# Optimization experiments

Hardware: AMD Instinct MI355X
Metric: run time of the kernel (lower is better)

The kernel has to match this reference:

```python
import jax, jax.numpy as jnp
import numpy as np

B, N, K, D, H = 8, 128, 64, 256, 8  # batch, groups, keys-per-query, k_dim (=h_size), n_head


def setup_inputs() -> dict:
    key = jax.random.key(0)
    kq, kk, kv, kw, kb = jax.random.split(key, 5)
    bound = 1.0 / np.sqrt(D)  # torch nn.Bilinear default init bound
    return {
        "q": jax.random.normal(kq, (B, N, 1, D), jnp.float32),
        "k": jax.random.normal(kk, (B, N, K, D), jnp.float32),
        "v": jax.random.normal(kv, (B, N, K, D), jnp.float32),
        "W": jax.random.uniform(kw, (H, D, D), jnp.float32, -bound, bound),
        "b": jax.random.uniform(kb, (H,), jnp.float32, -bound, bound),
    }


def reference(q, k, v, W, b):
    Bs, Ns, Ks, Ds = k.shape
    Hh = W.shape[0]
    qe = q[:, :, 0, :]  # (B,N,D); torch expands q over K, einsum broadcasts instead
    # nn.Bilinear: scores[b,n,k,h] = q[b,n,:] @ W[h] @ k[b,n,k,:] + b[h]
    scores = jnp.einsum('bnd,hde,bnke->bnkh', qe, W, k) + b  # (B,N,K,H)
    # Faithful to torch's .view(B, N, -1, K): row-major reinterpretation of the
    # trailing (K, H) pair as (H, K) — a dim-mixing reshape, not a transpose.
    attn = scores.reshape(Bs, Ns, Hh, Ks)
    attn = jax.nn.softmax(attn, axis=-1)  # softmax over last dim (dropout p=0)
    # matmul(attn, v) -> (B,N,H,Dv); then sum over the head axis
    output = jnp.einsum('bnhk,bnkd->bnd', attn, v)
    return output, attn
```

## Files before the change

### kernel.cpp

```cpp
#include <hip/hip_runtime.h>
#include <math.h>

namespace {

constexpr int D = 256;
constexpr int H = 8;

typedef __attribute__((ext_vector_type(8))) short bf16x8;
typedef __attribute__((ext_vector_type(4))) float f32x4;

__device__ inline unsigned short bf16rn(float x) {
  unsigned u = __builtin_bit_cast(unsigned, x);
  u += 0x7fffu + ((u >> 16) & 1u);
  return (unsigned short)(u >> 16);
}
__device__ inline float bf16tof(unsigned short b) {
  return __builtin_bit_cast(float, (unsigned)b << 16);
}

constexpr size_t OFF_QWB = 0;
constexpr size_t OFF_WFH = (size_t)8 << 20;
constexpr size_t OFF_WFL = (size_t)9 << 20;
constexpr size_t OFF_QFH = (size_t)10 << 20;
constexpr size_t OFF_QFL = ((size_t)10 << 20) + ((size_t)512 << 10);

__global__ __launch_bounds__(256) void prep_kernel(
    const float* __restrict__ q, const float* __restrict__ W,
    char* __restrict__ ws) {
  const int gid = blockIdx.x * 256 + threadIdx.x;
  float e[8];
  char *hi_base, *lo_base;
  size_t outoff;
  if (gid < 65536) {
    const int l = gid & 63, ks = (gid >> 6) & 7, he = gid >> 9;
    const int h = he >> 4, et = he & 15;
    const int d0 = ks * 32 + ((l >> 4) << 3);
    const int ecol = et * 16 + (l & 15);
    const float* src = W + (size_t)h * 65536 + (size_t)d0 * 256 + ecol;
    #pragma unroll
    for (int j = 0; j < 8; ++j) e[j] = src[j * 256];
    hi_base = ws + OFF_WFH; lo_base = ws + OFF_WFL;
    outoff = (size_t)gid * 16;
  } else {
    const int t = gid - 65536;
    const int l = t & 63, ks = (t >> 6) & 7, bt = t >> 9;
    const int row = bt * 16 + (l & 15);
    const int d0 = ks * 32 + ((l >> 4) << 3);
    const float4* src = reinterpret_cast<const float4*>(q + (size_t)row * 256 + d0);
    float4 a = src[0], b = src[1];
    e[0] = a.x; e[1] = a.y; e[2] = a.z; e[3] = a.w;
    e[4] = b.x; e[5] = b.y; e[6] = b.z; e[7] = b.w;
    hi_base = ws + OFF_QFH; lo_base = ws + OFF_QFL;
    outoff = (size_t)t * 16;
  }
  unsigned hw[4], lw[4];
  #pragma unroll
  for (int p = 0; p < 4; ++p) {
    unsigned short h0 = bf16rn(e[2 * p]), h1 = bf16rn(e[2 * p + 1]);
    unsigned short l0 = bf16rn(e[2 * p] - bf16tof(h0));
    unsigned short l1 = bf16rn(e[2 * p + 1] - bf16tof(h1));
    hw[p] = (unsigned)h0 | ((unsigned)h1 << 16);
    lw[p] = (unsigned)l0 | ((unsigned)l1 << 16);
  }
  *reinterpret_cast<uint4*>(hi_base + outoff) = make_uint4(hw[0], hw[1], hw[2], hw[3]);
  *reinterpret_cast<uint4*>(lo_base + outoff) = make_uint4(lw[0], lw[1], lw[2], lw[3]);
}

__global__ __launch_bounds__(256) void qw_mfma_kernel(
    const char* __restrict__ ws_in, unsigned short* __restrict__ qWb) {
  const int tid = threadIdx.x;
  const int w   = blockIdx.x * 4 + (tid >> 6);
  const int l   = tid & 63;
  const int bng = w >> 5;
  const int heg = w & 31;
  const char* qfh = ws_in + OFF_QFH;
  const char* qfl = ws_in + OFF_QFL;
  const char* wfh = ws_in + OFF_WFH;
  const char* wfl = ws_in + OFF_WFL;

  f32x4 acc[2][4];
  #pragma unroll
  for (int i = 0; i < 2; ++i)
    #pragma unroll
    for (int j = 0; j < 4; ++j) acc[i][j] = {0.f, 0.f, 0.f, 0.f};

  #pragma unroll 2
  for (int ks = 0; ks < 8; ++ks) {
    bf16x8 aH[2], aL[2], bH[4], bL[4];
    #pragma unroll
    for (int i = 0; i < 2; ++i) {
      const size_t off = ((size_t)((bng * 2 + i) * 8 + ks) * 64 + l) * 16;
      aH[i] = *reinterpret_cast<const bf16x8*>(qfh + off);
      aL[i] = *reinterpret_cast<const bf16x8*>(qfl + off);
    }
    #pragma unroll
    for (int j = 0; j < 4; ++j) {
      const size_t off = ((size_t)((heg * 4 + j) * 8 + ks) * 64 + l) * 16;
      bH[j] = *reinterpret_cast<const bf16x8*>(wfh + off);
      bL[j] = *reinterpret_cast<const bf16x8*>(wfl + off);
    }
    #pragma unroll
    for (int i = 0; i < 2; ++i)
      #pragma unroll
      for (int j = 0; j < 4; ++j) {
        acc[i][j] = __builtin_amdgcn_mfma_f32_16x16x32_bf16(aH[i], bH[j], acc[i][j], 0, 0, 0);
        acc[i][j] = __builtin_amdgcn_mfma_f32_16x16x32_bf16(aH[i], bL[j], acc[i][j], 0, 0, 0);
        acc[i][j] = __builtin_amdgcn_mfma_f32_16x16x32_bf16(aL[i], bH[j], acc[i][j], 0, 0, 0);
      }
  }

  const int rbase = (l >> 4) * 4;
  const int col   = l & 15;
  #pragma unroll
  for (int i = 0; i < 2; ++i)
    #pragma unroll
    for (int j = 0; j < 4; ++j) {
      const size_t cidx = (size_t)(heg * 4 + j) * 16 + col;
      #pragma unroll
      for (int r = 0; r < 4; ++r) {
        const int bn = (bng * 2 + i) * 16 + rbase + r;
        qWb[(size_t)bn * 2048 + cidx] = bf16rn(acc[i][j][r]);
      }
    }
}

constexpr int FB2   = 0;
constexpr int WSP2  = 8320;
constexpr int SMEM3 = 9344;

__global__ __launch_bounds__(256, 4) void attn_fused_kernel(
    const unsigned short* __restrict__ qWb, const float* __restrict__ kin,
    const float* __restrict__ vin, const float* __restrict__ bin,
    float* __restrict__ out, float* __restrict__ attn_out) {
  __shared__ alignas(16) long long smem_ll[SMEM3 / 8];
  char* sm = reinterpret_cast<char*>(smem_ll);
  float* wsp = reinterpret_cast<float*>(sm + WSP2);
  const int tid = threadIdx.x;
  const int bn  = blockIdx.x;
  const int wid = tid >> 6;
  const int ln  = tid & 63;

  const float* arow = kin + (size_t)bn * 16384 +
                      (size_t)(wid * 16 + (ln & 15)) * 256 + ((ln >> 4) << 3);
  float4 ka[16];
  #pragma unroll
  for (int ks = 0; ks < 8; ++ks) {
    ka[2 * ks]     = *reinterpret_cast<const float4*>(arow + ks * 32);
    ka[2 * ks + 1] = *reinterpret_cast<const float4*>(arow + ks * 32 + 4);
  }
  uint4 qh = *reinterpret_cast<const uint4*>(qWb + (size_t)bn * 2048 + tid * 8);

  {
    const int ks = tid >> 5, slot = 32 + (tid & 31);
    *reinterpret_cast<uint4*>(sm + FB2 + ks * 1040 + slot * 16) =
        make_uint4(0u, 0u, 0u, 0u);
  }
  #pragma unroll
  for (int i = 0; i < 2; ++i) {
    const int p = 2 * tid + i;
    const int hh = p >> 6, equad = p & 63;
    const int ks = equad >> 3, g = (equad >> 1) & 3, j0 = (equad & 1) * 4;
    const int base = FB2 + ks * 1040 + (hh * 4 + g) * 16 + j0 * 2;
    *reinterpret_cast<uint2*>(sm + base) =
        i == 0 ? make_uint2(qh.x, qh.y) : make_uint2(qh.z, qh.w);
  }
  __syncthreads();

  const int slot_r = (ln & 15) * 4 + (ln >> 4);
  const char* pbH = sm + FB2 + slot_r * 16;
  f32x4 acc = {0.f, 0.f, 0.f, 0.f};
  #pragma unroll
  for (int ks = 0; ks < 8; ++ks) {
    const float4 a0 = ka[2 * ks], a1 = ka[2 * ks + 1];
    bf16x8 aH;
    aH[0] = (short)bf16rn(a0.x); aH[1] = (short)bf16rn(a0.y);
    aH[2] = (short)bf16rn(a0.z); aH[3] = (short)bf16rn(a0.w);
    aH[4] = (short)bf16rn(a1.x); aH[5] = (short)bf16rn(a1.y);
    aH[6] = (short)bf16rn(a1.z); aH[7] = (short)bf16rn(a1.w);
    bf16x8 bH = *reinterpret_cast<const bf16x8*>(pbH + ks * 1040);
    acc = __builtin_amdgcn_mfma_f32_16x16x32_bf16(aH, bH, acc, 0, 0, 0);
  }

  const float bias = bin[ln & 7];
  const int col = ln & 15;
  const bool valid = col < 8;
  float x0 = acc[0] + bias, x1 = acc[1] + bias, x2 = acc[2] + bias, x3 = acc[3] + bias;
  float m = valid ? fmaxf(fmaxf(x0, x1), fmaxf(x2, x3)) : -1e30f;
  m = fmaxf(m, __shfl_xor(m, 1, 64));
  m = fmaxf(m, __shfl_xor(m, 2, 64));
  m = fmaxf(m, __shfl_xor(m, 4, 64));
  m = fmaxf(m, __shfl_xor(m, 16, 64));
  float e0 = valid ? expf(x0 - m) : 0.f;
  float e1 = valid ? expf(x1 - m) : 0.f;
  float e2 = valid ? expf(x2 - m) : 0.f;
  float e3 = valid ? expf(x3 - m) : 0.f;
  float s = e0 + e1 + e2 + e3;
  s += __shfl_xor(s, 1, 64);
  s += __shfl_xor(s, 2, 64);
  s += __shfl_xor(s, 4, 64);
  s += __shfl_xor(s, 16, 64);
  float inv = 1.f / s;
  float p0 = e0 * inv, p1 = e1 * inv, p2 = e2 * inv, p3 = e3 * inv;
  if (valid) {
    size_t base = (size_t)bn * 512 + (size_t)(wid * 16 + (ln >> 4) * 4) * 8 + col;
    attn_out[base]      = p0;
    attn_out[base + 8]  = p1;
    attn_out[base + 16] = p2;
    attn_out[base + 24] = p3;
  }
  p0 += __shfl_xor(p0, 32, 64);
  p1 += __shfl_xor(p1, 32, 64);
  p2 += __shfl_xor(p2, 32, 64);
  p3 += __shfl_xor(p3, 32, 64);
  if (ln < 32 && (ln & 15) < 8) {
    const int rb = (ln >> 4) * 4;
    const int c8 = ln & 7;
    float* w = wsp + wid * 64;
    w[(rb + 0) * 8 + c8] = p0;
    w[(rb + 1) * 8 + c8] = p1;
    w[(rb + 2) * 8 + c8] = p2;
    w[(rb + 3) * 8 + c8] = p3;
  }
  __syncthreads();

  const float4* v4 = reinterpret_cast<const float4*>(vin) + (size_t)bn * 4096;
  float4 av = make_float4(0.f, 0.f, 0.f, 0.f);
  #pragma unroll
  for (int i = 0; i < 16; ++i) {
    const int r = wid + 4 * i;
    float w = wsp[r] + wsp[64 + r] + wsp[128 + r] + wsp[192 + r];
    float4 vv = v4[r * 64 + ln];
    av.x += w * vv.x; av.y += w * vv.y; av.z += w * vv.z; av.w += w * vv.w;
  }
  float* s_red = reinterpret_cast<float*>(sm);
  *reinterpret_cast<float4*>(&s_red[wid * 260 + (ln << 2)]) = av;
  __syncthreads();

  out[(size_t)bn * D + tid] =
      s_red[tid] + s_red[260 + tid] + s_red[520 + tid] + s_red[780 + tid];
}

}

extern "C" void kernel_launch(void* const* d_in, const int* in_sizes, int n_in,
                              void* d_out, int out_size, void* d_ws, size_t ws_size,
                              hipStream_t stream) {
  const float* q = (const float*)d_in[0];
  const float* k = (const float*)d_in[1];
  const float* v = (const float*)d_in[2];
  const float* W = (const float*)d_in[3];
  const float* b = (const float*)d_in[4];

  float* out  = (float*)d_out;
  float* attn = out + 262144;
  char*  ws   = (char*)d_ws;
  unsigned short* qWb = (unsigned short*)(ws + OFF_QWB);

  hipLaunchKernelGGL(prep_kernel,       dim3(384),  dim3(256), 0, stream, q, W, ws);
  hipLaunchKernelGGL(qw_mfma_kernel,    dim3(256),  dim3(256), 0, stream, ws, qWb);
  hipLaunchKernelGGL(attn_fused_kernel, dim3(1024), dim3(256), 0, stream,
                     qWb, k, v, b, out, attn);
}
```

Baseline: 41.43 us.

## Fuse bf16 hi/lo split of q and W into the qW MFMA kernel

Removes the separate prep kernel that wrote bf16 hi/lo fragment layouts of q and W to the workspace. The MFMA kernel now loads fp32 q and W directly and splits them into hi/lo in registers, with a smaller per-wave tile (1x2 instead of 2x4) over a four-times larger grid. This saves one launch and a workspace round trip. In exchange, W is re-read and re-converted by many more waves, using strided scalar fp32 loads.

```diff
diff --git a/kernel.cpp b/kernel.cpp
--- a/kernel.cpp
+++ b/kernel.cpp
@@ -17,111 +17,72 @@
 __device__ inline float bf16tof(unsigned short b) {
   return __builtin_bit_cast(float, (unsigned)b << 16);
 }
-
-constexpr size_t OFF_QWB = 0;
-constexpr size_t OFF_WFH = (size_t)8 << 20;
-constexpr size_t OFF_WFL = (size_t)9 << 20;
-constexpr size_t OFF_QFH = (size_t)10 << 20;
-constexpr size_t OFF_QFL = ((size_t)10 << 20) + ((size_t)512 << 10);
-
-__global__ __launch_bounds__(256) void prep_kernel(
+__device__ inline void hilo8(const float* e, bf16x8& hv, bf16x8& lv) {
+  #pragma unroll
+  for (int p = 0; p < 8; ++p) {
+    unsigned short h = bf16rn(e[p]);
+    hv[p] = (short)h;
+    lv[p] = (short)bf16rn(e[p] - bf16tof(h));
+  }
+}
+
+__global__ __launch_bounds__(256) void qw_direct_kernel(
     const float* __restrict__ q, const float* __restrict__ W,
-    char* __restrict__ ws) {
-  const int gid = blockIdx.x * 256 + threadIdx.x;
-  float e[8];
-  char *hi_base, *lo_base;
-  size_t outoff;
-  if (gid < 65536) {
-    const int l = gid & 63, ks = (gid >> 6) & 7, he = gid >> 9;
-    const int h = he >> 4, et = he & 15;
-    const int d0 = ks * 32 + ((l >> 4) << 3);
-    const int ecol = et * 16 + (l & 15);
-    const float* src = W + (size_t)h * 65536 + (size_t)d0 * 256 + ecol;
-    #pragma unroll
-    for (int j = 0; j < 8; ++j) e[j] = src[j * 256];
-    hi_base = ws + OFF_WFH; lo_base = ws + OFF_WFL;
-    outoff = (size_t)gid * 16;
-  } else {
-    const int t = gid - 65536;
-    const int l = t & 63, ks = (t >> 6) & 7, bt = t >> 9;
-    const int row = bt * 16 + (l & 15);
-    const int d0 = ks * 32 + ((l >> 4) << 3);
-    const float4* src = reinterpret_cast<const float4*>(q + (size_t)row * 256 + d0);
-    float4 a = src[0], b = src[1];
-    e[0] = a.x; e[1] = a.y; e[2] = a.z; e[3] = a.w;
-    e[4] = b.x; e[5] = b.y; e[6] = b.z; e[7] = b.w;
-    hi_base = ws + OFF_QFH; lo_base = ws + OFF_QFL;
-    outoff = (size_t)t * 16;
-  }
-  unsigned hw[4], lw[4];
-  #pragma unroll
-  for (int p = 0; p < 4; ++p) {
-    unsigned short h0 = bf16rn(e[2 * p]), h1 = bf16rn(e[2 * p + 1]);
-    unsigned short l0 = bf16rn(e[2 * p] - bf16tof(h0));
-    unsigned short l1 = bf16rn(e[2 * p + 1] - bf16tof(h1));
-    hw[p] = (unsigned)h0 | ((unsigned)h1 << 16);
-    lw[p] = (unsigned)l0 | ((unsigned)l1 << 16);
-  }
-  *reinterpret_cast<uint4*>(hi_base + outoff) = make_uint4(hw[0], hw[1], hw[2], hw[3]);
-  *reinterpret_cast<uint4*>(lo_base + outoff) = make_uint4(lw[0], lw[1], lw[2], lw[3]);
-}
-
-__global__ __launch_bounds__(256) void qw_mfma_kernel(
-    const char* __restrict__ ws_in, unsigned short* __restrict__ qWb) {
+    unsigned short* __restrict__ qWb) {
   const int tid = threadIdx.x;
   const int w   = blockIdx.x * 4 + (tid >> 6);
   const int l   = tid & 63;
-  const int bng = w >> 5;
-  const int heg = w & 31;
-  const char* qfh = ws_in + OFF_QFH;
-  const char* qfl = ws_in + OFF_QFL;
-  const char* wfh = ws_in + OFF_WFH;
-  const char* wfl = ws_in + OFF_WFL;
-
-  f32x4 acc[2][4];
-  #pragma unroll
-  for (int i = 0; i < 2; ++i)
-    #pragma unroll
-    for (int j = 0; j < 4; ++j) acc[i][j] = {0.f, 0.f, 0.f, 0.f};
+  const int bt  = w >> 6;
+  const int hp  = w & 63;
+  const int lrow  = l & 15;
+  const int lcol8 = (l >> 4) << 3;
+
+  f32x4 acc[2];
+  acc[0] = f32x4{0.f, 0.f, 0.f, 0.f};
+  acc[1] = f32x4{0.f, 0.f, 0.f, 0.f};
+
+  const float* qbase = q + (size_t)(bt * 16 + lrow) * 256 + lcol8;
 
   #pragma unroll 2
   for (int ks = 0; ks < 8; ++ks) {
-    bf16x8 aH[2], aL[2], bH[4], bL[4];
+    float ea[8];
+    {
+      const float4 a0 = *reinterpret_cast<const float4*>(qbase + ks * 32);
+      const float4 a1 = *reinterpret_cast<const float4*>(qbase + ks * 32 + 4);
+      ea[0] = a0.x; ea[1] = a0.y; ea[2] = a0.z; ea[3] = a0.w;
+      ea[4] = a1.x; ea[5] = a1.y; ea[6] = a1.z; ea[7] = a1.w;
+    }
+    bf16x8 aH, aL;
+    hilo8(ea, aH, aL);
+
     #pragma unroll
-    for (int i = 0; i < 2; ++i) {
-      const size_t off = ((size_t)((bng * 2 + i) * 8 + ks) * 64 + l) * 16;
-      aH[i] = *reinterpret_cast<const bf16x8*>(qfh + off);
-      aL[i] = *reinterpret_cast<const bf16x8*>(qfl + off);
+    for (int j = 0; j < 2; ++j) {
+      const int he = hp * 2 + j;
+      const int h  = he >> 4, et = he & 15;
+      const float* wp = W + (size_t)h * 65536 +
+                        (size_t)(ks * 32 + lcol8) * 256 + et * 16 + lrow;
+      float eb[8];
+      #pragma unroll
+      for (int jj = 0; jj < 8; ++jj) eb[jj] = wp[(size_t)jj * 256];
+      bf16x8 bH, bL;
+      hilo8(eb, bH, bL);
+      acc[j] = __builtin_amdgcn_mfma_f32_16x16x32_bf16(aH, bH, acc[j], 0, 0, 0);
+      acc[j] = __builtin_amdgcn_mfma_f32_16x16x32_bf16(aH, bL, acc[j], 0, 0, 0);
+      acc[j] = __builtin_amdgcn_mfma_f32_16x16x32_bf16(aL, bH, acc[j], 0, 0, 0);
     }
-    #pragma unroll
-    for (int j = 0; j < 4; ++j) {
-      const size_t off = ((size_t)((heg * 4 + j) * 8 + ks) * 64 + l) * 16;
-      bH[j] = *reinterpret_cast<const bf16x8*>(wfh + off);
-      bL[j] = *reinterpret_cast<const bf16x8*>(wfl + off);
-    }
-    #pragma unroll
-    for (int i = 0; i < 2; ++i)
-      #pragma unroll
-      for (int j = 0; j < 4; ++j) {
-        acc[i][j] = __builtin_amdgcn_mfma_f32_16x16x32_bf16(aH[i], bH[j], acc[i][j], 0, 0, 0);
-        acc[i][j] = __builtin_amdgcn_mfma_f32_16x16x32_bf16(aH[i], bL[j], acc[i][j], 0, 0, 0);
-        acc[i][j] = __builtin_amdgcn_mfma_f32_16x16x32_bf16(aL[i], bH[j], acc[i][j], 0, 0, 0);
-      }
   }
 
   const int rbase = (l >> 4) * 4;
   const int col   = l & 15;
   #pragma unroll
-  for (int i = 0; i < 2; ++i)
+  for (int j = 0; j < 2; ++j) {
+    const size_t cidx = (size_t)(hp * 2 + j) * 16 + col;
     #pragma unroll
-    for (int j = 0; j < 4; ++j) {
-      const size_t cidx = (size_t)(heg * 4 + j) * 16 + col;
-      #pragma unroll
-      for (int r = 0; r < 4; ++r) {
-        const int bn = (bng * 2 + i) * 16 + rbase + r;
-        qWb[(size_t)bn * 2048 + cidx] = bf16rn(acc[i][j][r]);
-      }
+    for (int r = 0; r < 4; ++r) {
+      const int bn = bt * 16 + rbase + r;
+      qWb[(size_t)bn * 2048 + cidx] = bf16rn(acc[j][r]);
     }
+  }
 }
 
 constexpr int FB2   = 0;
@@ -253,11 +214,9 @@
 
   float* out  = (float*)d_out;
   float* attn = out + 262144;
-  char*  ws   = (char*)d_ws;
-  unsigned short* qWb = (unsigned short*)(ws + OFF_QWB);
-
-  hipLaunchKernelGGL(prep_kernel,       dim3(384),  dim3(256), 0, stream, q, W, ws);
-  hipLaunchKernelGGL(qw_mfma_kernel,    dim3(256),  dim3(256), 0, stream, ws, qWb);
+  unsigned short* qWb = (unsigned short*)d_ws;
+
+  hipLaunchKernelGGL(qw_direct_kernel,  dim3(1024), dim3(256), 0, stream, q, W, qWb);
   hipLaunchKernelGGL(attn_fused_kernel, dim3(1024), dim3(256), 0, stream,
                      qWb, k, v, b, out, attn);
 }
```

Result: no change. 41.41 us (-0.1%).
